# Kernel tuning notes

Hardware: AMD Instinct MI355X
Metric: run time of the kernel (lower is better)

The kernel has to match this reference:

```python
import jax, jax.numpy as jnp
import numpy as np

N = 100000        # n_total_nodes
D = 64            # embed_dim
E = 1600000       # nnz of A_in (avg degree 16)
OFFSET = 20000    # ENTITY_OFFSET (== n_users)
DIMS = [64, 64, 32]  # conv_dim_list with input dim prepended


def _xavier(key, shape):
    fan_in, fan_out = shape[-1], shape[-2] if len(shape) > 1 else shape[-1]
    lim = jnp.sqrt(6.0 / (fan_in + fan_out))
    return jax.random.uniform(key, shape, minval=-lim, maxval=lim, dtype=jnp.float32)


def _l2norm(x, eps=1e-12):
    return x / jnp.maximum(jnp.linalg.norm(x, axis=-1, keepdims=True), eps)


def setup_inputs() -> dict:
    key = jax.random.key(0)
    ks = jax.random.split(key, 20)
    inp = {
        "user_ids": jax.random.randint(ks[0], (1024,), 0, OFFSET),
        "item_ids": jax.random.randint(ks[1], (4096,), 0, N),
        "aux_info_all": jax.random.uniform(ks[2], (N, 3), dtype=jnp.float32),
        "A_rows": jax.random.randint(ks[3], (E,), 0, N),
        "A_cols": jax.random.randint(ks[4], (E,), 0, N),
        "A_vals": jax.random.uniform(ks[5], (E,), dtype=jnp.float32) / 16.0,
        "entity_embed": _xavier(ks[6], (N, D)),
        "type_embed": _xavier(ks[7], (2, D)),
        "W_aux": _xavier(ks[8], (D, 3)),
        "b_aux": jnp.zeros((D,), jnp.float32),
        "W1_0": _xavier(ks[9], (DIMS[1], DIMS[0])),
        "b1_0": jnp.zeros((DIMS[1],), jnp.float32),
        "W2_0": _xavier(ks[10], (DIMS[1], DIMS[0])),
        "b2_0": jnp.zeros((DIMS[1],), jnp.float32),
        "W1_1": _xavier(ks[11], (DIMS[2], DIMS[1])),
        "b1_1": jnp.zeros((DIMS[2],), jnp.float32),
        "W2_1": _xavier(ks[12], (DIMS[2], DIMS[1])),
        "b2_1": jnp.zeros((DIMS[2],), jnp.float32),
    }
    return inp


def reference(user_ids, item_ids, aux_info_all, A_rows, A_cols, A_vals,
              entity_embed, type_embed, W_aux, b_aux,
              W1_0, b1_0, W2_0, b2_0, W1_1, b1_1, W2_1, b2_1):
    # holographic_fusion over the full table (eval mode: dropout is identity)
    gate = jax.nn.sigmoid(jnp.log1p(aux_info_all) @ W_aux.T + b_aux) * 0.15 + 1.0
    ego = _l2norm(entity_embed * gate)
    type_labels = (jnp.arange(N) >= OFFSET).astype(jnp.int32)
    ego = ego + type_embed[type_labels]

    all_embed = [ego]
    for (W1, b1, W2, b2) in [(W1_0, b1_0, W2_0, b2_0), (W1_1, b1_1, W2_1, b2_1)]:
        # sparse A_in @ ego  (COO SpMM via gather + segment_sum)
        side = jax.ops.segment_sum(A_vals[:, None] * ego[A_cols], A_rows,
                                   num_segments=N)
        sum_emb = jax.nn.leaky_relu((ego + side) @ W1.T + b1, negative_slope=0.01)
        bi_emb = jax.nn.leaky_relu((ego * side) @ W2.T + b2, negative_slope=0.01)
        ego = sum_emb + bi_emb
        all_embed.append(_l2norm(ego))

    all_e = jnp.concatenate(all_embed, axis=1)  # [N, 64+64+32]
    # calc_score: user x item similarity
    return all_e[user_ids] @ all_e[item_ids].T
```

## Files before the change

### kernel.cpp

```cpp
#include <hip/hip_runtime.h>
#include <math.h>

#define NN 100000
#define DIM 64
#define ENT_OFFSET 20000
#define BSH 7
#define NBK 782
#define TILE_C 8192
#define CAPD 8192
#define HPAD 68
#define SRP 168

typedef _Float16 f16;
typedef _Float16 f16x2 __attribute__((ext_vector_type(2)));
typedef _Float16 f16x4 __attribute__((ext_vector_type(4)));
typedef _Float16 f16x8 __attribute__((ext_vector_type(8)));
typedef float f32x4 __attribute__((ext_vector_type(4)));

#if __has_builtin(__builtin_amdgcn_fdot2)
__device__ inline float FDOT2(f16x2 a, f16x2 b, float c) {
    return __builtin_amdgcn_fdot2(a, b, c, false);
}
#else
__device__ inline float FDOT2(f16x2 a, f16x2 b, float c) {
    return c + (float)a.x * (float)b.x + (float)a.y * (float)b.y;
}
#endif

__global__ void fuse_kernel(const float* __restrict__ aux,
                            const float* __restrict__ entity,
                            const float* __restrict__ type_emb,
                            const float* __restrict__ W_aux,
                            const float* __restrict__ b_aux,
                            f16* __restrict__ alle,
                            f16* __restrict__ e0c)
{
    int n    = blockIdx.x * 4 + (threadIdx.x >> 6);
    int lane = threadIdx.x & 63;

    float la = 0.0f;
    if (lane < 3) la = __logf(1.0f + aux[n * 3 + lane]);
    float a0 = __shfl(la, 0);
    float a1 = __shfl(la, 1);
    float a2 = __shfl(la, 2);

    float g = fmaf(a0, W_aux[lane * 3 + 0],
              fmaf(a1, W_aux[lane * 3 + 1],
              fmaf(a2, W_aux[lane * 3 + 2], b_aux[lane])));
    float eneg = __expf(-g);
    g = __builtin_amdgcn_rcpf(1.0f + eneg) * 0.15f + 1.0f;

    float v  = entity[n * 64 + lane] * g;
    float ss = v * v;
    #pragma unroll
    for (int m = 32; m >= 1; m >>= 1) ss += __shfl_xor(ss, m);
    v = v * rsqrtf(fmaxf(ss, 1e-24f));
    v += type_emb[(n >= ENT_OFFSET ? 1 : 0) * 64 + lane];

    f16 h = (f16)v;
    alle[(size_t)n * 160 + lane] = h;
    e0c[(size_t)n * 64 + lane]   = h;
}

__global__ void mark_ids(const int* __restrict__ uids, int nu,
                         const int* __restrict__ iids, int ni,
                         int* __restrict__ f0, int* __restrict__ f1)
{
    int i = blockIdx.x * blockDim.x + threadIdx.x;
    if (i >= nu + ni) return;
    int r = (i < nu) ? uids[i] : iids[i - nu];
    f1[r] = 1;
    f0[r] = 1;
}

__global__ void mark_edges(const int* __restrict__ rows, const int* __restrict__ cols,
                           int E, const int* __restrict__ f1, int* __restrict__ f0)
{
    int i = blockIdx.x * blockDim.x + threadIdx.x;
    int s = gridDim.x * blockDim.x;
    for (; i < E; i += s)
        if (f1[rows[i]]) f0[cols[i]] = 1;
}

__global__ __launch_bounds__(256) void compact_kernel(const int* __restrict__ flags,
                                                      int* __restrict__ list,
                                                      int* __restrict__ cnt)
{
    __shared__ int lds[256];
    __shared__ int base;
    int tid = threadIdx.x;
    int i = blockIdx.x * 256 + tid;
    int f = (i < NN) ? flags[i] : 0;
    lds[tid] = f;
    __syncthreads();
    for (int off = 1; off < 256; off <<= 1) {
        int v = (tid >= off) ? lds[tid - off] : 0;
        __syncthreads();
        lds[tid] += v;
        __syncthreads();
    }
    if (tid == 255) {
        int total = lds[255];
        base = total ? atomicAdd(cnt, total) : 0;
    }
    __syncthreads();
    if (f) list[base + lds[tid] - 1] = i;
}

__global__ void bucket_hist(const int* __restrict__ rows, int E,
                            const int* __restrict__ f0, int* __restrict__ bcnt)
{
    __shared__ int lh[NBK];
    for (int b = threadIdx.x; b < NBK; b += blockDim.x) lh[b] = 0;
    __syncthreads();
    int i = blockIdx.x * blockDim.x + threadIdx.x;
    int s = gridDim.x * blockDim.x;
    for (; i < E; i += s) {
        int r = rows[i];
        if (f0[r]) atomicAdd(&lh[r >> BSH], 1);
    }
    __syncthreads();
    for (int b = threadIdx.x; b < NBK; b += blockDim.x)
        if (lh[b]) atomicAdd(&bcnt[b], lh[b]);
}

__global__ __launch_bounds__(1024) void bucket_scan(const int* __restrict__ bcnt,
                                                    int* __restrict__ bstart,
                                                    int* __restrict__ bfill,
                                                    int* __restrict__ rowptr)
{
    __shared__ int lds[1024];
    int t = threadIdx.x;
    int v = (t < NBK) ? bcnt[t] : 0;
    lds[t] = v;
    __syncthreads();
    for (int off = 1; off < 1024; off <<= 1) {
        int u = (t >= off) ? lds[t - off] : 0;
        __syncthreads();
        lds[t] += u;
        __syncthreads();
    }
    if (t < NBK) { bstart[t + 1] = lds[t]; bfill[t] = 0; }
    if (t == 0)  { bstart[0] = 0; }
    if (t == NBK - 1) rowptr[NN] = lds[t];
}

__global__ __launch_bounds__(1024) void bucket_scatter(
    const int* __restrict__ rows, const int* __restrict__ cols,
    const float* __restrict__ vals, int E, const int* __restrict__ f0,
    const int* __restrict__ bstart, int* __restrict__ bfill,
    uint2* __restrict__ cv)
{
    __shared__ int lhist[NBK];
    __shared__ int gpos[NBK];
    int tid   = threadIdx.x;
    int gbase = blockIdx.x * TILE_C;
    int n     = min(TILE_C, E - gbase);

    for (int b = tid; b < NBK; b += 1024) lhist[b] = 0;
    __syncthreads();
    for (int i = tid; i < n; i += 1024) {
        int r = rows[gbase + i];
        if (f0[r]) atomicAdd(&lhist[r >> BSH], 1);
    }
    __syncthreads();
    for (int b = tid; b < NBK; b += 1024) {
        int c = lhist[b];
        if (c > 0) gpos[b] = bstart[b] + atomicAdd(&bfill[b], c);
        lhist[b] = 0;
    }
    __syncthreads();
    for (int i = tid; i < n; i += 1024) {
        int r = rows[gbase + i];
        if (!f0[r]) continue;
        int b = r >> BSH;
        int ofs = atomicAdd(&lhist[b], 1);
        unsigned meta = (unsigned)cols[gbase + i] | ((unsigned)(r & 127) << 17);
        cv[gpos[b] + ofs] = make_uint2(meta, __float_as_uint(vals[gbase + i]));
    }
}

__global__ __launch_bounds__(256) void bucket_sort(
    const int* __restrict__ bstart, uint2* __restrict__ cv, int* __restrict__ rowptr)
{
    __shared__ uint2 raw[CAPD];
    __shared__ int hist[128], excl[128], fill[128];
    int b = blockIdx.x, tid = threadIdx.x;
    int base = bstart[b];
    int count = bstart[b + 1] - base;

    if (tid < 128) { hist[tid] = 0; fill[tid] = 0; }
    __syncthreads();
    for (int i = tid; i < count && i < CAPD; i += 256) {
        uint2 e = cv[base + i];
        raw[i] = e;
        atomicAdd(&hist[(e.x >> 17) & 127], 1);
    }
    __syncthreads();
    if (tid < 128) excl[tid] = hist[tid];
    __syncthreads();
    for (int off = 1; off < 128; off <<= 1) {
        int v = (tid < 128 && tid >= off) ? excl[tid - off] : 0;
        __syncthreads();
        if (tid < 128) excl[tid] += v;
        __syncthreads();
    }
    if (tid < 128) {
        int ex = excl[tid] - hist[tid];
        excl[tid] = ex;
        int g = (b << BSH) + tid;
        if (g < NN) rowptr[g] = base + ex;
    }
    __syncthreads();
    for (int i = tid; i < count && i < CAPD; i += 256) {
        uint2 e = raw[i];
        int lr = (e.x >> 17) & 127;
        int ofs = excl[lr] + atomicAdd(&fill[lr], 1);
        cv[base + ofs] = make_uint2(e.x & 0x1FFFF, e.y);
    }
}

template <int STR>
__global__ __launch_bounds__(256) void spmm_csr_list(
    const int* __restrict__ rowptr, const uint2* __restrict__ cv,
    const f16* __restrict__ x, f16* __restrict__ side,
    const int* __restrict__ list, const int* __restrict__ cnt)
{
    int wid = (blockIdx.x * blockDim.x + threadIdx.x) >> 6;
    if (wid >= *cnt) return;
    int r = list[wid];
    int lane = threadIdx.x & 63;
    int s = rowptr[r], e = rowptr[r + 1];

    float acc = 0.0f;
    int i = s;
    for (; i + 8 <= e; i += 8) {
        uint2 e0 = cv[i],     e1 = cv[i + 1], e2 = cv[i + 2], e3 = cv[i + 3];
        uint2 e4 = cv[i + 4], e5 = cv[i + 5], e6 = cv[i + 6], e7 = cv[i + 7];
        float x0 = (float)x[(size_t)e0.x * STR + lane];
        float x1 = (float)x[(size_t)e1.x * STR + lane];
        float x2 = (float)x[(size_t)e2.x * STR + lane];
        float x3 = (float)x[(size_t)e3.x * STR + lane];
        float x4 = (float)x[(size_t)e4.x * STR + lane];
        float x5 = (float)x[(size_t)e5.x * STR + lane];
        float x6 = (float)x[(size_t)e6.x * STR + lane];
        float x7 = (float)x[(size_t)e7.x * STR + lane];
        acc += __uint_as_float(e0.y) * x0 + __uint_as_float(e1.y) * x1
             + __uint_as_float(e2.y) * x2 + __uint_as_float(e3.y) * x3
             + __uint_as_float(e4.y) * x4 + __uint_as_float(e5.y) * x5
             + __uint_as_float(e6.y) * x6 + __uint_as_float(e7.y) * x7;
    }
    for (; i < e; i++) {
        uint2 e0 = cv[i];
        acc += __uint_as_float(e0.y) * (float)x[(size_t)e0.x * STR + lane];
    }
    side[r * 64 + lane] = (f16)acc;
}

template <int OUT, int XSTR, bool WRITE_RAW>
__global__ __launch_bounds__(256) void layer_kernel(
    const f16* __restrict__ x,
    const f16* __restrict__ side,
    const float* __restrict__ W1, const float* __restrict__ b1,
    const float* __restrict__ W2, const float* __restrict__ b2,
    f16* __restrict__ out_norm,
    f16* __restrict__ out_raw,
    const int* __restrict__ list, const int* __restrict__ cnt)
{
    constexpr int OPT = OUT / 8;
    __shared__ f16 W1h[OUT * HPAD];
    __shared__ f16 W2h[OUT * HPAD];
    __shared__ f16 s_sum[64 * HPAD];
    __shared__ f16 s_bi [64 * HPAD];

    int tid  = threadIdx.x;
    int n0   = blockIdx.x * 64;
    int cntv = *cnt;
    if (n0 >= cntv) return;

    for (int t = tid; t < OUT * 64; t += 256) {
        int r = t >> 6, c = t & 63;
        W1h[r * HPAD + c] = (f16)W1[t];
        W2h[r * HPAD + c] = (f16)W2[t];
    }
    for (int t = tid; t < 64 * 16; t += 256) {
        int n = t >> 4, q = t & 15;
        int li = n0 + n;
        f16x4 xe = {0,0,0,0}, sd = {0,0,0,0};
        if (li < cntv) {
            int gn = list[li];
            xe = *(const f16x4*)&x[(size_t)gn * XSTR + q * 4];
            sd = *(const f16x4*)&side[(size_t)gn * 64 + q * 4];
        }
        f16x4 sm, bi;
        #pragma unroll
        for (int k = 0; k < 4; k++) {
            float xf = (float)xe[k], sf = (float)sd[k];
            sm[k] = (f16)(xf + sf);
            bi[k] = (f16)(xf * sf);
        }
        *(f16x4*)&s_sum[n * HPAD + q * 4] = sm;
        *(f16x4*)&s_bi [n * HPAD + q * 4] = bi;
    }
    __syncthreads();

    int og = tid & 7;
    int nb = tid >> 3;
    int nA = nb * 2, nB = nA + 1;

    float acc1[2][OPT], acc2[2][OPT];
    #pragma unroll
    for (int i = 0; i < OPT; i++) {
        int o = og + 8 * i;
        acc1[0][i] = b1[o]; acc1[1][i] = b1[o];
        acc2[0][i] = b2[o]; acc2[1][i] = b2[o];
    }

    #pragma unroll 4
    for (int d4 = 0; d4 < 16; d4++) {
        f16x4 sA = *(const f16x4*)&s_sum[nA * HPAD + d4 * 4];
        f16x4 bA = *(const f16x4*)&s_bi [nA * HPAD + d4 * 4];
        f16x4 sB = *(const f16x4*)&s_sum[nB * HPAD + d4 * 4];
        f16x4 bB = *(const f16x4*)&s_bi [nB * HPAD + d4 * 4];
        f16x2 sA0 = {sA[0], sA[1]}, sA1 = {sA[2], sA[3]};
        f16x2 bA0 = {bA[0], bA[1]}, bA1 = {bA[2], bA[3]};
        f16x2 sB0 = {sB[0], sB[1]}, sB1 = {sB[2], sB[3]};
        f16x2 bB0 = {bB[0], bB[1]}, bB1 = {bB[2], bB[3]};
        #pragma unroll
        for (int i = 0; i < OPT; i++) {
            int o = og + 8 * i;
            f16x4 w1 = *(const f16x4*)&W1h[o * HPAD + d4 * 4];
            f16x4 w2 = *(const f16x4*)&W2h[o * HPAD + d4 * 4];
            f16x2 w10 = {w1[0], w1[1]}, w11 = {w1[2], w1[3]};
            f16x2 w20 = {w2[0], w2[1]}, w21 = {w2[2], w2[3]};
            acc1[0][i] = FDOT2(sA1, w11, FDOT2(sA0, w10, acc1[0][i]));
            acc1[1][i] = FDOT2(sB1, w11, FDOT2(sB0, w10, acc1[1][i]));
            acc2[0][i] = FDOT2(bA1, w21, FDOT2(bA0, w20, acc2[0][i]));
            acc2[1][i] = FDOT2(bB1, w21, FDOT2(bB0, w20, acc2[1][i]));
        }
    }

    float eo[2][OPT];
    float ss0 = 0.0f, ss1 = 0.0f;
    #pragma unroll
    for (int i = 0; i < OPT; i++) {
        float a = acc1[0][i]; a = a > 0.0f ? a : 0.01f * a;
        float c = acc2[0][i]; c = c > 0.0f ? c : 0.01f * c;
        eo[0][i] = a + c; ss0 += eo[0][i] * eo[0][i];
        a = acc1[1][i]; a = a > 0.0f ? a : 0.01f * a;
        c = acc2[1][i]; c = c > 0.0f ? c : 0.01f * c;
        eo[1][i] = a + c; ss1 += eo[1][i] * eo[1][i];
    }
    #pragma unroll
    for (int m = 1; m <= 4; m <<= 1) {
        ss0 += __shfl_xor(ss0, m);
        ss1 += __shfl_xor(ss1, m);
    }
    float inv0 = rsqrtf(fmaxf(ss0, 1e-24f));
    float inv1 = rsqrtf(fmaxf(ss1, 1e-24f));

    int liA = n0 + nA, liB = n0 + nB;
    int gnA = (liA < cntv) ? list[liA] : -1;
    int gnB = (liB < cntv) ? list[liB] : -1;
    #pragma unroll
    for (int i = 0; i < OPT; i++) {
        int o = og + 8 * i;
        if (gnA >= 0) {
            out_norm[(size_t)gnA * 160 + o] = (f16)(eo[0][i] * inv0);
            if (WRITE_RAW) out_raw[(size_t)gnA * 64 + o] = (f16)eo[0][i];
        }
        if (gnB >= 0) {
            out_norm[(size_t)gnB * 160 + o] = (f16)(eo[1][i] * inv1);
            if (WRITE_RAW) out_raw[(size_t)gnB * 64 + o] = (f16)eo[1][i];
        }
    }
}

__global__ __launch_bounds__(256) void score_kernel(
    const f16* __restrict__ alle,
    const int* __restrict__ uids, const int* __restrict__ iids,
    float* __restrict__ out, int n_items)
{
    __shared__ f16 Us[64 * SRP];
    __shared__ f16 Vs[64 * SRP];
    int tid = threadIdx.x;
    int i0 = blockIdx.y * 64, j0 = blockIdx.x * 64;

    for (int t = tid; t < 64 * 20; t += 256) {
        int r = t / 20, c = t % 20;
        int uid = uids[i0 + r];
        int iid = iids[j0 + r];
        *(f16x8*)&Us[r * SRP + c * 8] = *(const f16x8*)&alle[(size_t)uid * 160 + c * 8];
        *(f16x8*)&Vs[r * SRP + c * 8] = *(const f16x8*)&alle[(size_t)iid * 160 + c * 8];
    }
    __syncthreads();

    int w = tid >> 6, lane = tid & 63;
    int wr = (w >> 1) * 32, wc = (w & 1) * 32;
    int lr = lane & 15, lk = (lane >> 4) * 8;

    f32x4 acc00 = {0,0,0,0}, acc01 = {0,0,0,0}, acc10 = {0,0,0,0}, acc11 = {0,0,0,0};
    #pragma unroll
    for (int kc = 0; kc < 160; kc += 32) {
        f16x8 a0 = *(const f16x8*)&Us[(wr +      lr) * SRP + kc + lk];
        f16x8 a1 = *(const f16x8*)&Us[(wr + 16 + lr) * SRP + kc + lk];
        f16x8 b0 = *(const f16x8*)&Vs[(wc +      lr) * SRP + kc + lk];
        f16x8 b1 = *(const f16x8*)&Vs[(wc + 16 + lr) * SRP + kc + lk];
        acc00 = __builtin_amdgcn_mfma_f32_16x16x32_f16(a0, b0, acc00, 0, 0, 0);
        acc01 = __builtin_amdgcn_mfma_f32_16x16x32_f16(a0, b1, acc01, 0, 0, 0);
        acc10 = __builtin_amdgcn_mfma_f32_16x16x32_f16(a1, b0, acc10, 0, 0, 0);
        acc11 = __builtin_amdgcn_mfma_f32_16x16x32_f16(a1, b1, acc11, 0, 0, 0);
    }

    int orow = (lane >> 4) * 4, ocol = lane & 15;
    #pragma unroll
    for (int r = 0; r < 4; r++) {
        int iA = i0 + wr + orow + r;
        int iB = i0 + wr + 16 + orow + r;
        out[(size_t)iA * n_items + j0 + wc +      ocol] = acc00[r];
        out[(size_t)iA * n_items + j0 + wc + 16 + ocol] = acc01[r];
        out[(size_t)iB * n_items + j0 + wc +      ocol] = acc10[r];
        out[(size_t)iB * n_items + j0 + wc + 16 + ocol] = acc11[r];
    }
}

extern "C" void kernel_launch(void* const* d_in, const int* in_sizes, int n_in,
                              void* d_out, int out_size, void* d_ws, size_t ws_size,
                              hipStream_t stream) {
    const int*   user_ids = (const int*)  d_in[0];
    const int*   item_ids = (const int*)  d_in[1];
    const float* aux      = (const float*)d_in[2];
    const int*   A_rows   = (const int*)  d_in[3];
    const int*   A_cols   = (const int*)  d_in[4];
    const float* A_vals   = (const float*)d_in[5];
    const float* entity   = (const float*)d_in[6];
    const float* type_emb = (const float*)d_in[7];
    const float* W_aux    = (const float*)d_in[8];
    const float* b_aux    = (const float*)d_in[9];
    const float* W1_0     = (const float*)d_in[10];
    const float* b1_0     = (const float*)d_in[11];
    const float* W2_0     = (const float*)d_in[12];
    const float* b2_0     = (const float*)d_in[13];
    const float* W1_1     = (const float*)d_in[14];
    const float* b1_1     = (const float*)d_in[15];
    const float* W2_1     = (const float*)d_in[16];
    const float* b2_1     = (const float*)d_in[17];

    int E       = in_sizes[3];
    int n_users = in_sizes[0];
    int n_items = in_sizes[1];

    char* ws = (char*)d_ws;
    size_t off = 0;
    f16*   alle   = (f16*)  (ws + off); off += (size_t)NN * 160 * 2;
    f16*   e0c    = (f16*)  (ws + off); off += (size_t)NN * 64 * 2;
    f16*   e1raw  = (f16*)  (ws + off); off += (size_t)NN * 64 * 2;
    f16*   side   = (f16*)  (ws + off); off += (size_t)NN * 64 * 2;
    uint2* cv     = (uint2*)(ws + off); off += (size_t)E * 8;
    int*   rowptr = (int*)  (ws + off); off += (size_t)(NN + 1) * 4;
    int*   bstart = (int*)  (ws + off); off += (size_t)(NBK + 1) * 4;
    int*   bfill  = (int*)  (ws + off); off += (size_t)NBK * 4;
    int*   L0     = (int*)  (ws + off); off += (size_t)NN * 4;
    int*   L1     = (int*)  (ws + off); off += (size_t)NN * 4;
    char*  zbase  = ws + off;
    int*   bcnt   = (int*)  (ws + off); off += (size_t)NBK * 4;
    int*   f0     = (int*)  (ws + off); off += (size_t)NN * 4;
    int*   f1     = (int*)  (ws + off); off += (size_t)NN * 4;
    int*   cnt0   = (int*)  (ws + off); off += 4;
    int*   cnt1   = (int*)  (ws + off); off += 4;
    size_t zbytes = (size_t)(NBK + 2 * NN + 2) * 4;

    hipMemsetAsync(zbase, 0, zbytes, stream);

    int nid = n_users + n_items;
    mark_ids<<<(nid + 255) / 256, 256, 0, stream>>>(user_ids, n_users,
                                                    item_ids, n_items, f0, f1);
    mark_edges<<<2048, 256, 0, stream>>>(A_rows, A_cols, E, f1, f0);
    compact_kernel<<<(NN + 255) / 256, 256, 0, stream>>>(f0, L0, cnt0);
    compact_kernel<<<(NN + 255) / 256, 256, 0, stream>>>(f1, L1, cnt1);

    bucket_hist<<<512, 256, 0, stream>>>(A_rows, E, f0, bcnt);
    bucket_scan<<<1, 1024, 0, stream>>>(bcnt, bstart, bfill, rowptr);
    bucket_scatter<<<(E + TILE_C - 1) / TILE_C, 1024, 0, stream>>>(
        A_rows, A_cols, A_vals, E, f0, bstart, bfill, cv);
    bucket_sort<<<NBK, 256, 0, stream>>>(bstart, cv, rowptr);

    fuse_kernel<<<NN / 4, 256, 0, stream>>>(aux, entity, type_emb, W_aux, b_aux,
                                            alle, e0c);

    int sgrid_rows = (NN + 3) / 4;
    int lgrid      = (NN + 63) / 64;

    spmm_csr_list<64><<<sgrid_rows, 256, 0, stream>>>(rowptr, cv, e0c, side, L0, cnt0);
    layer_kernel<64, 64, true><<<lgrid, 256, 0, stream>>>(e0c, side,
                                                          W1_0, b1_0, W2_0, b2_0,
                                                          alle + 64, e1raw, L0, cnt0);

    spmm_csr_list<64><<<sgrid_rows, 256, 0, stream>>>(rowptr, cv, e1raw, side, L1, cnt1);
    layer_kernel<32, 64, false><<<lgrid, 256, 0, stream>>>(e1raw, side,
                                                           W1_1, b1_1, W2_1, b2_1,
                                                           alle + 128, nullptr, L1, cnt1);

    dim3 sgrid(n_items / 64, n_users / 64);
    score_kernel<<<sgrid, 256, 0, stream>>>(alle, user_ids, item_ids,
                                            (float*)d_out, n_items);
}
```

Measured before the change: 212.9 us.

## Drop duplicate layer-0 copy, deepen SpMM gather unroll, halve scatter tile

The fuse kernel no longer writes layer-0 embeddings into the concatenated 160-wide table. The score kernel now reads layer 0 from e0c and layers 1-2 from a new 96-wide buffer, which removes 100000x64 half-precision stores. The SpMM loop issues 16 independent gathers per iteration with a 4-wide tail, giving more memory-level parallelism at the cost of more registers. The scatter tile and capacity constants are halved, which doubles the number of bucket_scatter blocks.

```diff
diff --git a/kernel.cpp b/kernel.cpp
--- a/kernel.cpp
+++ b/kernel.cpp
@@ -6,8 +6,8 @@
 #define ENT_OFFSET 20000
 #define BSH 7
 #define NBK 782
-#define TILE_C 8192
-#define CAPD 8192
+#define TILE_C 4096
+#define CAPD 4096
 #define HPAD 68
 #define SRP 168
 
@@ -32,7 +32,6 @@
                             const float* __restrict__ type_emb,
                             const float* __restrict__ W_aux,
                             const float* __restrict__ b_aux,
-                            f16* __restrict__ alle,
                             f16* __restrict__ e0c)
 {
     int n    = blockIdx.x * 4 + (threadIdx.x >> 6);
@@ -57,9 +56,7 @@
     v = v * rsqrtf(fmaxf(ss, 1e-24f));
     v += type_emb[(n >= ENT_OFFSET ? 1 : 0) * 64 + lane];
 
-    f16 h = (f16)v;
-    alle[(size_t)n * 160 + lane] = h;
-    e0c[(size_t)n * 64 + lane]   = h;
+    e0c[(size_t)n * 64 + lane] = (f16)v;
 }
 
 __global__ void mark_ids(const int* __restrict__ uids, int nu,
@@ -234,21 +231,26 @@
 
     float acc = 0.0f;
     int i = s;
-    for (; i + 8 <= e; i += 8) {
-        uint2 e0 = cv[i],     e1 = cv[i + 1], e2 = cv[i + 2], e3 = cv[i + 3];
-        uint2 e4 = cv[i + 4], e5 = cv[i + 5], e6 = cv[i + 6], e7 = cv[i + 7];
+    for (; i + 16 <= e; i += 16) {
+        uint2 ce[16];
+        float xv[16];
+        #pragma unroll
+        for (int k = 0; k < 16; k++) ce[k] = cv[i + k];
+        #pragma unroll
+        for (int k = 0; k < 16; k++)
+            xv[k] = (float)x[(size_t)ce[k].x * STR + lane];
+        #pragma unroll
+        for (int k = 0; k < 16; k++)
+            acc = fmaf(__uint_as_float(ce[k].y), xv[k], acc);
+    }
+    for (; i + 4 <= e; i += 4) {
+        uint2 e0 = cv[i], e1 = cv[i + 1], e2 = cv[i + 2], e3 = cv[i + 3];
         float x0 = (float)x[(size_t)e0.x * STR + lane];
         float x1 = (float)x[(size_t)e1.x * STR + lane];
         float x2 = (float)x[(size_t)e2.x * STR + lane];
         float x3 = (float)x[(size_t)e3.x * STR + lane];
-        float x4 = (float)x[(size_t)e4.x * STR + lane];
-        float x5 = (float)x[(size_t)e5.x * STR + lane];
-        float x6 = (float)x[(size_t)e6.x * STR + lane];
-        float x7 = (float)x[(size_t)e7.x * STR + lane];
         acc += __uint_as_float(e0.y) * x0 + __uint_as_float(e1.y) * x1
-             + __uint_as_float(e2.y) * x2 + __uint_as_float(e3.y) * x3
-             + __uint_as_float(e4.y) * x4 + __uint_as_float(e5.y) * x5
-             + __uint_as_float(e6.y) * x6 + __uint_as_float(e7.y) * x7;
+             + __uint_as_float(e2.y) * x2 + __uint_as_float(e3.y) * x3;
     }
     for (; i < e; i++) {
         uint2 e0 = cv[i];
@@ -257,7 +259,7 @@
     side[r * 64 + lane] = (f16)acc;
 }
 
-template <int OUT, int XSTR, bool WRITE_RAW>
+template <int OUT, int XSTR, int OSTR, bool WRITE_RAW>
 __global__ __launch_bounds__(256) void layer_kernel(
     const f16* __restrict__ x,
     const f16* __restrict__ side,
@@ -366,18 +368,18 @@
     for (int i = 0; i < OPT; i++) {
         int o = og + 8 * i;
         if (gnA >= 0) {
-            out_norm[(size_t)gnA * 160 + o] = (f16)(eo[0][i] * inv0);
+            out_norm[(size_t)gnA * OSTR + o] = (f16)(eo[0][i] * inv0);
             if (WRITE_RAW) out_raw[(size_t)gnA * 64 + o] = (f16)eo[0][i];
         }
         if (gnB >= 0) {
-            out_norm[(size_t)gnB * 160 + o] = (f16)(eo[1][i] * inv1);
+            out_norm[(size_t)gnB * OSTR + o] = (f16)(eo[1][i] * inv1);
             if (WRITE_RAW) out_raw[(size_t)gnB * 64 + o] = (f16)eo[1][i];
         }
     }
 }
 
 __global__ __launch_bounds__(256) void score_kernel(
-    const f16* __restrict__ alle,
+    const f16* __restrict__ e0c, const f16* __restrict__ e12,
     const int* __restrict__ uids, const int* __restrict__ iids,
     float* __restrict__ out, int n_items)
 {
@@ -390,8 +392,16 @@
         int r = t / 20, c = t % 20;
         int uid = uids[i0 + r];
         int iid = iids[j0 + r];
-        *(f16x8*)&Us[r * SRP + c * 8] = *(const f16x8*)&alle[(size_t)uid * 160 + c * 8];
-        *(f16x8*)&Vs[r * SRP + c * 8] = *(const f16x8*)&alle[(size_t)iid * 160 + c * 8];
+        f16x8 u, v;
+        if (c < 8) {
+            u = *(const f16x8*)&e0c[(size_t)uid * 64 + c * 8];
+            v = *(const f16x8*)&e0c[(size_t)iid * 64 + c * 8];
+        } else {
+            u = *(const f16x8*)&e12[(size_t)uid * 96 + (c - 8) * 8];
+            v = *(const f16x8*)&e12[(size_t)iid * 96 + (c - 8) * 8];
+        }
+        *(f16x8*)&Us[r * SRP + c * 8] = u;
+        *(f16x8*)&Vs[r * SRP + c * 8] = v;
     }
     __syncthreads();
 
@@ -452,8 +462,8 @@
 
     char* ws = (char*)d_ws;
     size_t off = 0;
-    f16*   alle   = (f16*)  (ws + off); off += (size_t)NN * 160 * 2;
     f16*   e0c    = (f16*)  (ws + off); off += (size_t)NN * 64 * 2;
+    f16*   e12    = (f16*)  (ws + off); off += (size_t)NN * 96 * 2;
     f16*   e1raw  = (f16*)  (ws + off); off += (size_t)NN * 64 * 2;
     f16*   side   = (f16*)  (ws + off); off += (size_t)NN * 64 * 2;
     uint2* cv     = (uint2*)(ws + off); off += (size_t)E * 8;
@@ -485,23 +495,22 @@
         A_rows, A_cols, A_vals, E, f0, bstart, bfill, cv);
     bucket_sort<<<NBK, 256, 0, stream>>>(bstart, cv, rowptr);
 
-    fuse_kernel<<<NN / 4, 256, 0, stream>>>(aux, entity, type_emb, W_aux, b_aux,
-                                            alle, e0c);
+    fuse_kernel<<<NN / 4, 256, 0, stream>>>(aux, entity, type_emb, W_aux, b_aux, e0c);
 
     int sgrid_rows = (NN + 3) / 4;
     int lgrid      = (NN + 63) / 64;
 
     spmm_csr_list<64><<<sgrid_rows, 256, 0, stream>>>(rowptr, cv, e0c, side, L0, cnt0);
-    layer_kernel<64, 64, true><<<lgrid, 256, 0, stream>>>(e0c, side,
-                                                          W1_0, b1_0, W2_0, b2_0,
-                                                          alle + 64, e1raw, L0, cnt0);
+    layer_kernel<64, 64, 96, true><<<lgrid, 256, 0, stream>>>(e0c, side,
+                                                              W1_0, b1_0, W2_0, b2_0,
+                                                              e12, e1raw, L0, cnt0);
 
     spmm_csr_list<64><<<sgrid_rows, 256, 0, stream>>>(rowptr, cv, e1raw, side, L1, cnt1);
-    layer_kernel<32, 64, false><<<lgrid, 256, 0, stream>>>(e1raw, side,
-                                                           W1_1, b1_1, W2_1, b2_1,
-                                                           alle + 128, nullptr, L1, cnt1);
+    layer_kernel<32, 64, 96, false><<<lgrid, 256, 0, stream>>>(e1raw, side,
+                                                               W1_1, b1_1, W2_1, b2_1,
+                                                               e12 + 64, nullptr, L1, cnt1);
 
     dim3 sgrid(n_items / 64, n_users / 64);
-    score_kernel<<<sgrid, 256, 0, stream>>>(alle, user_ids, item_ids,
+    score_kernel<<<sgrid, 256, 0, stream>>>(e0c, e12, user_ids, item_ids,
                                             (float*)d_out, n_items);
 }
```

Measured after the change: 219.4 us. 3.1% more time.
